# Optimization experiments

Hardware: AMD Instinct MI355X
Metric: run time of the kernel (lower is better)

Reference implementation:

```python
import jax, jax.numpy as jnp
import numpy as np
from jax import lax

D_MODEL = 1024
N_HEADS = 16
HEAD_DIM = D_MODEL // N_HEADS
B, S = 4, 2048
EPS = 1e-5


def setup_inputs() -> dict:
    key = jax.random.key(0)
    ks = jax.random.split(key, 8)
    sc = 1.0 / np.sqrt(D_MODEL)
    return {
        "x": jax.random.normal(ks[0], (B, S, D_MODEL), dtype=jnp.float32),
        "Wq": jax.random.normal(ks[1], (D_MODEL, D_MODEL), dtype=jnp.float32) * sc,
        "Wk": jax.random.normal(ks[2], (D_MODEL, D_MODEL), dtype=jnp.float32) * sc,
        "Wv": jax.random.normal(ks[3], (D_MODEL, D_MODEL), dtype=jnp.float32) * sc,
        "Wa": jax.random.normal(ks[4], (D_MODEL, N_HEADS), dtype=jnp.float32) * sc,
        "ba": jnp.zeros((N_HEADS,), dtype=jnp.float32),
        "Wb": jax.random.normal(ks[5], (D_MODEL, N_HEADS), dtype=jnp.float32) * sc,
        "bb": jnp.zeros((N_HEADS,), dtype=jnp.float32),
        "Wg": jax.random.normal(ks[6], (D_MODEL, D_MODEL), dtype=jnp.float32) * sc,
        "Wo": jax.random.normal(ks[7], (D_MODEL, D_MODEL), dtype=jnp.float32) * sc,
        "g_norm": jnp.ones((D_MODEL,), dtype=jnp.float32),
    }


def _l2_normalize(v, eps=1e-12):
    # F.normalize(dim=-1) in float32
    v32 = v.astype(jnp.float32)
    n = jnp.sqrt(jnp.sum(v32 * v32, axis=-1, keepdims=True))
    return (v32 / jnp.maximum(n, eps)).astype(v.dtype)


def _rmsnorm(x, w):
    x32 = x.astype(jnp.float32)
    rms = lax.rsqrt(jnp.mean(x32 * x32, axis=-1, keepdims=True) + EPS)
    return (x32 * rms).astype(x.dtype) * w


def reference(x, Wq, Wk, Wv, Wa, ba, Wb, bb, Wg, Wo, g_norm):
    batch, seq_len, d_model = x.shape
    H, hd = N_HEADS, HEAD_DIM
    residual_input = x

    # projections -> [B, S, H, hd]
    q = (x @ Wq).reshape(batch, seq_len, H, hd)
    k = (x @ Wk).reshape(batch, seq_len, H, hd)
    v = (x @ Wv).reshape(batch, seq_len, H, hd)
    q = _l2_normalize(q)
    k = _l2_normalize(k)

    alpha = jax.nn.sigmoid(x @ Wa + ba)  # [B, S, H]
    beta = jax.nn.sigmoid(x @ Wb + bb)   # [B, S, H]

    # time-major for scan: [S, B, H, ...]
    qt = jnp.moveaxis(q, 1, 0)
    kt = jnp.moveaxis(k, 1, 0)
    vt = jnp.moveaxis(v, 1, 0)
    at = jnp.moveaxis(alpha, 1, 0)
    bt = jnp.moveaxis(beta, 1, 0)

    state0 = jnp.zeros((batch, H, hd, hd), dtype=x.dtype)

    def step(state, inp):
        q_t, k_t, v_t, a_t, b_t = inp  # [B,H,hd], [B,H]
        pred = jnp.einsum('bhde,bhd->bhe', state, k_t)
        error = v_t - pred
        update = jnp.einsum('bhe,bhd->bhde', b_t[..., None] * error, k_t)
        state = a_t[..., None, None] * state + update
        out = jnp.einsum('bhde,bhd->bhe', state, q_t)
        return state, out

    _, ys = lax.scan(step, state0, (qt, kt, vt, at, bt))  # ys: [S,B,H,hd]
    y = jnp.moveaxis(ys, 0, 1).reshape(batch, seq_len, d_model)

    gate = jax.nn.silu(residual_input @ Wg)
    y = _rmsnorm(y, g_norm) * gate
    return y @ Wo


if __name__ == "__main__":
    out = reference(**setup_inputs())
    print(out.shape)
```

## Files before the change

kernel.cpp:

```cpp
#include <hip/hip_runtime.h>
#include <hip/hip_bf16.h>
#include <math.h>

typedef __attribute__((ext_vector_type(8))) short bf16x8s;
typedef __attribute__((ext_vector_type(4))) float f32x4;

#define SEQ 2048
#define NTOK 8192
#define NQKV 3200

static __device__ __forceinline__ float bf2f(unsigned short u) {
  union { unsigned int i; float f; } c; c.i = ((unsigned int)u) << 16; return c.f;
}
static __device__ __forceinline__ unsigned short f2bf(float f) {
  union { float f; unsigned int i; } c; c.f = f;
  unsigned int x = c.i;
  return (unsigned short)((x + 0x7FFFu + ((x >> 16) & 1u)) >> 16);
}

static __device__ __forceinline__ float red8(float x) {
  union { float f; int i; } c, d;
  c.f = x; d.i = __builtin_amdgcn_update_dpp(0, c.i, 0xB1, 0xF, 0xF, true); x += d.f;
  c.f = x; d.i = __builtin_amdgcn_update_dpp(0, c.i, 0x4E, 0xF, 0xF, true); x += d.f;
  c.f = x; d.i = __builtin_amdgcn_update_dpp(0, c.i, 0x141, 0xF, 0xF, true); x += d.f;
  return x;
}
static __device__ __forceinline__ float red16(float x) {
  union { float f; int i; } c, d;
  c.f = x; d.i = __builtin_amdgcn_update_dpp(0, c.i, 0xB1, 0xF, 0xF, true); x += d.f;
  c.f = x; d.i = __builtin_amdgcn_update_dpp(0, c.i, 0x4E, 0xF, 0xF, true); x += d.f;
  c.f = x; d.i = __builtin_amdgcn_update_dpp(0, c.i, 0x141, 0xF, 0xF, true); x += d.f;
  c.f = x; d.i = __builtin_amdgcn_update_dpp(0, c.i, 0x140, 0xF, 0xF, true); x += d.f;
  return x;
}

__global__ __launch_bounds__(256) void castx_k(const float* __restrict__ in,
                                               unsigned short* __restrict__ out, int n4) {
  int i = blockIdx.x * 256 + threadIdx.x;
  if (i >= n4) return;
  float4 v = ((const float4*)in)[i];
  ushort4 o;
  o.x = f2bf(v.x); o.y = f2bf(v.y); o.z = f2bf(v.z); o.w = f2bf(v.w);
  ((ushort4*)out)[i] = o;
}

__global__ void transpose_k(const float* __restrict__ in,
                            unsigned short* __restrict__ out, int R, int C) {
  __shared__ unsigned short tile[32][33];
  int c0 = blockIdx.x * 32, r0 = blockIdx.y * 32;
  int tx = threadIdx.x, ty = threadIdx.y;
  for (int i = ty; i < 32; i += 8)
    tile[i][tx] = f2bf(in[(size_t)(r0 + i) * C + c0 + tx]);
  __syncthreads();
  for (int i = ty; i < 32; i += 8)
    out[(size_t)(c0 + i) * R + r0 + tx] = tile[tx][i];
}

__global__ void build_wabT(const float* __restrict__ Wa,
                           const float* __restrict__ Wb,
                           unsigned short* __restrict__ rows) {
  int i = blockIdx.x * 256 + threadIdx.x;
  int j = i >> 10, k = i & 1023;
  float v = 0.f;
  if (j < 16) v = Wa[k * 16 + j];
  else if (j < 32) v = Wb[k * 16 + (j - 16)];
  rows[(size_t)j * 1024 + k] = f2bf(v);
}

template<int MODE>
__global__ __launch_bounds__(256) void gemm_bt(const unsigned short* __restrict__ A,
                                               const unsigned short* __restrict__ Bt,
                                               void* __restrict__ Cv,
                                               int M, int N, int K,
                                               const float* __restrict__ ba,
                                               const float* __restrict__ bbp,
                                               float* __restrict__ alphaF,
                                               float* __restrict__ betaF) {
  __shared__ __align__(16) unsigned short As[128 * 32];
  __shared__ __align__(16) unsigned short Bs[128 * 32];
  int tiles_n = N >> 7;
  int tm = blockIdx.x / tiles_n, tn = blockIdx.x % tiles_n;
  int m0 = tm << 7, n0 = tn << 7;
  int tid = threadIdx.x;
  int wave = tid >> 6, lane = tid & 63;
  int wm = wave >> 1, wn = wave & 1;
  int r = lane & 15, qd = lane >> 4;
  int lr = lane >> 2, lc = lane & 3;

  f32x4 acc[4][4];
#pragma unroll
  for (int mi = 0; mi < 4; mi++)
#pragma unroll
    for (int ni = 0; ni < 4; ni++) acc[mi][ni] = (f32x4){0.f, 0.f, 0.f, 0.f};

  for (int k0 = 0; k0 < K; k0 += 32) {
#pragma unroll
    for (int gi = 0; gi < 2; ++gi) {
      int g = wave + gi * 4;
      int row = g * 16 + lr;
      const unsigned short* ga = A + (size_t)(m0 + row) * K + k0 + lc * 8;
      const unsigned short* gb = Bt + (size_t)(n0 + row) * K + k0 + lc * 8;
      __builtin_amdgcn_global_load_lds(
          (const __attribute__((address_space(1))) unsigned int*)ga,
          (__attribute__((address_space(3))) unsigned int*)(As + g * 512 + lane * 8),
          16, 0, 0);
      __builtin_amdgcn_global_load_lds(
          (const __attribute__((address_space(1))) unsigned int*)gb,
          (__attribute__((address_space(3))) unsigned int*)(Bs + g * 512 + lane * 8),
          16, 0, 0);
    }
    __syncthreads();
    bf16x8s af[4], bfr[4];
#pragma unroll
    for (int mi = 0; mi < 4; mi++)
      af[mi] = *(const bf16x8s*)&As[(wm * 64 + mi * 16 + r) * 32 + qd * 8];
#pragma unroll
    for (int ni = 0; ni < 4; ni++)
      bfr[ni] = *(const bf16x8s*)&Bs[(wn * 64 + ni * 16 + r) * 32 + qd * 8];
#pragma unroll
    for (int mi = 0; mi < 4; mi++)
#pragma unroll
      for (int ni = 0; ni < 4; ni++)
        acc[mi][ni] = __builtin_amdgcn_mfma_f32_16x16x32_bf16(af[mi], bfr[ni], acc[mi][ni], 0, 0, 0);
    __syncthreads();
  }

  bool qk = (MODE == 2) && (n0 < 2048);
#pragma unroll
  for (int mi = 0; mi < 4; mi++) {
    f32x4 sc = (f32x4){1.f, 1.f, 1.f, 1.f};
    if (qk) {
      f32x4 ss = acc[mi][0] * acc[mi][0] + acc[mi][1] * acc[mi][1]
               + acc[mi][2] * acc[mi][2] + acc[mi][3] * acc[mi][3];
#pragma unroll
      for (int cc = 0; cc < 4; cc++) {
        float s = red16(ss[cc]);
        sc[cc] = 1.f / fmaxf(sqrtf(s), 1e-12f);
      }
    }
#pragma unroll
    for (int ni = 0; ni < 4; ni++)
#pragma unroll
      for (int reg = 0; reg < 4; reg++) {
        int m = m0 + wm * 64 + mi * 16 + qd * 4 + reg;
        int n = n0 + wn * 64 + ni * 16 + r;
        float a = acc[mi][ni][reg];
        if (MODE == 0) ((unsigned short*)Cv)[(size_t)m * N + n] = f2bf(a);
        else if (MODE == 1) ((float*)Cv)[(size_t)m * N + n] = a;
        else {
          if (qk) a *= sc[reg];
          if (n < 3072) ((unsigned short*)Cv)[(size_t)m * 3072 + n] = f2bf(a);
          else if (n < 3104) {
            int j = n - 3072;
            float bias = (j < 16) ? ba[j] : bbp[j - 16];
            float s = 1.f / (1.f + expf(-(a + bias)));
            if (j < 16) alphaF[(size_t)m * 16 + j] = s;
            else        betaF[(size_t)m * 16 + (j - 16)] = s;
          }
        }
      }
  }
}

#define TC 32
#define NCH (SEQ / TC)
#define LK 0
#define LQ 2048
#define LV 4096
#define LABQ 4352
#define SBUF 4480

static __device__ __forceinline__ void unpack8(uint4 v, float* f) {
  f[0] = bf2f((unsigned short)(v.x & 0xffff)); f[1] = bf2f((unsigned short)(v.x >> 16));
  f[2] = bf2f((unsigned short)(v.y & 0xffff)); f[3] = bf2f((unsigned short)(v.y >> 16));
  f[4] = bf2f((unsigned short)(v.z & 0xffff)); f[5] = bf2f((unsigned short)(v.z >> 16));
  f[6] = bf2f((unsigned short)(v.w & 0xffff)); f[7] = bf2f((unsigned short)(v.w >> 16));
}

struct Pref { uint4 k8[4], q8[4], v8; float ab; };

static __device__ __forceinline__ Pref scan_load(const unsigned short* __restrict__ qkv,
                                                 const float* __restrict__ alphaF,
                                                 const float* __restrict__ betaF,
                                                 int b, int h, int ec, int t0, int tid) {
  Pref p; p.v8 = (uint4){0, 0, 0, 0};
  const unsigned short* base = qkv + (size_t)(b * SEQ + t0) * 3072 + h * 64;
#pragma unroll
  for (int j = 0; j < 4; ++j) {
    int idx = j * 64 + tid;
    int t = idx >> 3, seg = idx & 7;
    p.q8[j] = *(const uint4*)(base + (size_t)t * 3072 + seg * 8);
    p.k8[j] = *(const uint4*)(base + (size_t)t * 3072 + 1024 + seg * 8);
  }
  if (tid < 32) {
    p.v8 = *(const uint4*)(base + (size_t)tid * 3072 + 2048 + ec * 8);
    p.ab = alphaF[(size_t)(b * SEQ + t0 + tid) * 16 + h];
  } else {
    p.ab = betaF[(size_t)(b * SEQ + t0 + (tid - 32)) * 16 + h];
  }
  return p;
}

static __device__ __forceinline__ void scan_store(float* __restrict__ buf, const Pref& p, int tid) {
#pragma unroll
  for (int j = 0; j < 4; ++j) {
    int idx = j * 64 + tid;
    int t = idx >> 3, seg = idx & 7;
    float kf[8], qf[8];
    unpack8(p.k8[j], kf);
    unpack8(p.q8[j], qf);
    *(float4*)&buf[LK + t * 64 + seg * 8]     = (float4){kf[0], kf[1], kf[2], kf[3]};
    *(float4*)&buf[LK + t * 64 + seg * 8 + 4] = (float4){kf[4], kf[5], kf[6], kf[7]};
    *(float4*)&buf[LQ + t * 64 + seg * 8]     = (float4){qf[0], qf[1], qf[2], qf[3]};
    *(float4*)&buf[LQ + t * 64 + seg * 8 + 4] = (float4){qf[4], qf[5], qf[6], qf[7]};
    float s = kf[0]*qf[0] + kf[1]*qf[1] + kf[2]*qf[2] + kf[3]*qf[3]
            + kf[4]*qf[4] + kf[5]*qf[5] + kf[6]*qf[6] + kf[7]*qf[7];
    s = red8(s);
    if ((tid & 7) == 0) buf[LABQ + t * 4 + 2] = s;
  }
  if (tid < 32) {
    float vf[8];
    unpack8(p.v8, vf);
    *(float4*)&buf[LV + tid * 8]     = (float4){vf[0], vf[1], vf[2], vf[3]};
    *(float4*)&buf[LV + tid * 8 + 4] = (float4){vf[4], vf[5], vf[6], vf[7]};
    buf[LABQ + tid * 4 + 0] = p.ab;
  } else {
    buf[LABQ + (tid - 32) * 4 + 1] = p.ab;
  }
}

__global__ __launch_bounds__(64) void scan_k(const unsigned short* __restrict__ qkv,
                                             const float* __restrict__ alphaF,
                                             const float* __restrict__ betaF,
                                             unsigned short* __restrict__ y) {
  __shared__ float sm[2 * SBUF];
  int bh = blockIdx.x >> 3, ec = blockIdx.x & 7;
  int b = bh >> 4, h = bh & 15;
  int tid = threadIdx.x;
  int el = tid >> 3, g = tid & 3 + 0;
  g = tid & 7;

  float S0 = 0.f, S1 = 0.f, S2 = 0.f, S3 = 0.f;
  float S4 = 0.f, S5 = 0.f, S6 = 0.f, S7 = 0.f;

  Pref p = scan_load(qkv, alphaF, betaF, b, h, ec, 0, tid);
  scan_store(sm, p, tid);
  __syncthreads();

  unsigned short* yb = y + (size_t)(b * SEQ) * 1024 + h * 64 + ec * 8 + el;

  for (int c = 0; c < NCH; ++c) {
    if (c + 1 < NCH)
      p = scan_load(qkv, alphaF, betaF, b, h, ec, (c + 1) * TC, tid);

    const float* bb = sm + (c & 1) * SBUF;
    float4 rk0[2], rk1[2], rq0[2], rq1[2], rabq[2];
    float rve[2];
#pragma unroll
    for (int i = 0; i < 2; ++i) {
      rk0[i] = *(const float4*)&bb[LK + i * 64 + g * 8];
      rk1[i] = *(const float4*)&bb[LK + i * 64 + g * 8 + 4];
      rq0[i] = *(const float4*)&bb[LQ + i * 64 + g * 8];
      rq1[i] = *(const float4*)&bb[LQ + i * 64 + g * 8 + 4];
      rve[i] = bb[LV + i * 8 + el];
      rabq[i] = *(const float4*)&bb[LABQ + i * 4];
    }
    float yo[TC];
#pragma unroll
    for (int t = 0; t < TC; ++t) {
      const int sl = t & 1;
      float4 k0 = rk0[sl], k1 = rk1[sl], q0 = rq0[sl], q1 = rq1[sl];
      float4 abq = rabq[sl];
      float ve = rve[sl];
      float at = abq.x, bt = abq.y, kqv = abq.z;
      float btve = bt * ve;
      float pr = ((S0*k0.x + S1*k0.y) + (S2*k0.z + S3*k0.w))
               + ((S4*k1.x + S5*k1.y) + (S6*k1.z + S7*k1.w));
      float qs = ((S0*q0.x + S1*q0.y) + (S2*q0.z + S3*q0.w))
               + ((S4*q1.x + S5*q1.y) + (S6*q1.z + S7*q1.w));
      pr = red8(pr);
      qs = red8(qs);
      float be = btve - bt * pr;
      S0 = at*S0 + be*k0.x;  S1 = at*S1 + be*k0.y;
      S2 = at*S2 + be*k0.z;  S3 = at*S3 + be*k0.w;
      S4 = at*S4 + be*k1.x;  S5 = at*S5 + be*k1.y;
      S6 = at*S6 + be*k1.z;  S7 = at*S7 + be*k1.w;
      yo[t] = at * qs + be * kqv;
      if (t + 2 < TC) {
        const int tn = t + 2;
        rk0[sl] = *(const float4*)&bb[LK + tn * 64 + g * 8];
        rk1[sl] = *(const float4*)&bb[LK + tn * 64 + g * 8 + 4];
        rq0[sl] = *(const float4*)&bb[LQ + tn * 64 + g * 8];
        rq1[sl] = *(const float4*)&bb[LQ + tn * 64 + g * 8 + 4];
        rve[sl] = bb[LV + tn * 8 + el];
        rabq[sl] = *(const float4*)&bb[LABQ + tn * 4];
      }
    }
    if (g == 0) {
#pragma unroll
      for (int t = 0; t < TC; ++t)
        yb[(size_t)(c * TC + t) * 1024] = f2bf(yo[t]);
    }
    if (c + 1 < NCH) {
      scan_store(sm + ((c + 1) & 1) * SBUF, p, tid);
      __syncthreads();
    }
  }
}

__global__ __launch_bounds__(256) void rmsgate_k(const unsigned short* __restrict__ y,
                                                 const unsigned short* __restrict__ gl,
                                                 const float* __restrict__ gnorm,
                                                 unsigned short* __restrict__ z) {
  __shared__ float red[4];
  int row = blockIdx.x, tid = threadIdx.x;
  size_t base = (size_t)row * 1024 + tid * 4;
  uint2 yv = *(const uint2*)&y[base];
  float f0 = bf2f((unsigned short)(yv.x & 0xffff)), f1 = bf2f((unsigned short)(yv.x >> 16));
  float f2 = bf2f((unsigned short)(yv.y & 0xffff)), f3 = bf2f((unsigned short)(yv.y >> 16));
  float ss = f0 * f0 + f1 * f1 + f2 * f2 + f3 * f3;
#pragma unroll
  for (int s = 1; s < 64; s <<= 1) ss += __shfl_xor(ss, s);
  if ((tid & 63) == 0) red[tid >> 6] = ss;
  __syncthreads();
  ss = red[0] + red[1] + red[2] + red[3];
  float rms = rsqrtf(ss * (1.0f / 1024.0f) + 1e-5f);
  uint2 gv = *(const uint2*)&gl[base];
  float4 gn = *(const float4*)&gnorm[tid * 4];
  float g[4] = {bf2f((unsigned short)(gv.x & 0xffff)), bf2f((unsigned short)(gv.x >> 16)),
                bf2f((unsigned short)(gv.y & 0xffff)), bf2f((unsigned short)(gv.y >> 16))};
  float gnv[4] = {gn.x, gn.y, gn.z, gn.w};
  float fv[4] = {f0, f1, f2, f3};
  unsigned short o[4];
#pragma unroll
  for (int jj = 0; jj < 4; jj++) {
    float gate = g[jj] / (1.f + expf(-g[jj]));
    o[jj] = f2bf(fv[jj] * rms * gnv[jj] * gate);
  }
  uint2 ov;
  ov.x = (unsigned int)o[0] | ((unsigned int)o[1] << 16);
  ov.y = (unsigned int)o[2] | ((unsigned int)o[3] << 16);
  *(uint2*)&z[base] = ov;
}

extern "C" void kernel_launch(void* const* d_in, const int* in_sizes, int n_in,
                              void* d_out, int out_size, void* d_ws, size_t ws_size,
                              hipStream_t stream) {
  const float* x     = (const float*)d_in[0];
  const float* Wq    = (const float*)d_in[1];
  const float* Wk    = (const float*)d_in[2];
  const float* Wv    = (const float*)d_in[3];
  const float* Wa    = (const float*)d_in[4];
  const float* ba    = (const float*)d_in[5];
  const float* Wb    = (const float*)d_in[6];
  const float* bb    = (const float*)d_in[7];
  const float* Wg    = (const float*)d_in[8];
  const float* Wo    = (const float*)d_in[9];
  const float* gnorm = (const float*)d_in[10];
  float* out = (float*)d_out;

  unsigned short* xbf    = (unsigned short*)d_ws;
  unsigned short* Bt_qkv = xbf + (size_t)NTOK * 1024;
  unsigned short* Bt_g   = Bt_qkv + (size_t)NQKV * 1024;
  unsigned short* Bt_o   = Bt_g + (size_t)1024 * 1024;
  unsigned short* qkv    = Bt_o + (size_t)1024 * 1024;
  unsigned short* gatelin= qkv + (size_t)NTOK * 3072;
  unsigned short* ybuf   = gatelin + (size_t)NTOK * 1024;
  float* alphaF          = (float*)(ybuf + (size_t)NTOK * 1024);
  float* betaF           = alphaF + (size_t)NTOK * 16;
  unsigned short* zbuf   = xbf;

  castx_k<<<NTOK * 1024 / 4 / 256, 256, 0, stream>>>(x, xbf, NTOK * 1024 / 4);
  dim3 tb(32, 8);
  transpose_k<<<dim3(32, 32), tb, 0, stream>>>(Wq, Bt_qkv, 1024, 1024);
  transpose_k<<<dim3(32, 32), tb, 0, stream>>>(Wk, Bt_qkv + (size_t)1024 * 1024, 1024, 1024);
  transpose_k<<<dim3(32, 32), tb, 0, stream>>>(Wv, Bt_qkv + (size_t)2048 * 1024, 1024, 1024);
  transpose_k<<<dim3(32, 32), tb, 0, stream>>>(Wg, Bt_g, 1024, 1024);
  transpose_k<<<dim3(32, 32), tb, 0, stream>>>(Wo, Bt_o, 1024, 1024);
  build_wabT<<<512, 256, 0, stream>>>(Wa, Wb, Bt_qkv + (size_t)3072 * 1024);

  gemm_bt<2><<<(NTOK / 128) * (NQKV / 128), 256, 0, stream>>>(
      xbf, Bt_qkv, qkv, NTOK, NQKV, 1024, ba, bb, alphaF, betaF);
  gemm_bt<0><<<(NTOK / 128) * (1024 / 128), 256, 0, stream>>>(
      xbf, Bt_g, gatelin, NTOK, 1024, 1024, nullptr, nullptr, nullptr, nullptr);
  scan_k<<<512, 64, 0, stream>>>(qkv, alphaF, betaF, ybuf);
  rmsgate_k<<<NTOK, 256, 0, stream>>>(ybuf, gatelin, gnorm, zbuf);
  gemm_bt<1><<<(NTOK / 128) * (1024 / 128), 256, 0, stream>>>(
      zbuf, Bt_o, out, NTOK, 1024, 1024, nullptr, nullptr, nullptr, nullptr);
}
```

Measured before the change: 614.6 us.

## Lookahead-restructure delta-rule scan to take reductions off the recurrence critical path

Rewrites the per-step recurrence so the state-times-k and state-times-q dot products for step t+1 are computed from the state before step t's update. They are then corrected using precomputed k_{t}·k_{t+1} and k_{t}·q_{t+1} scalars. This lets the cross-lane DPP reductions overlap with the state update instead of serializing it. It also folds beta into v when staging, packs the state into float2 vectors to allow packed FMA, and precomputes the extra dot products in shared memory, which needs an extra barrier and slightly larger buffers. The algebra introduces small floating-point reassociation differences.

```diff
diff --git a/kernel.cpp b/kernel.cpp
--- a/kernel.cpp
+++ b/kernel.cpp
@@ -4,6 +4,7 @@
 
 typedef __attribute__((ext_vector_type(8))) short bf16x8s;
 typedef __attribute__((ext_vector_type(4))) float f32x4;
+typedef __attribute__((ext_vector_type(2))) float f32x2;
 
 #define SEQ 2048
 #define NTOK 8192
@@ -168,7 +169,7 @@
 #define LQ 2048
 #define LV 4096
 #define LABQ 4352
-#define SBUF 4480
+#define SBUF 4608
 
 static __device__ __forceinline__ void unpack8(uint4 v, float* f) {
   f[0] = bf2f((unsigned short)(v.x & 0xffff)); f[1] = bf2f((unsigned short)(v.x >> 16));
@@ -199,6 +200,20 @@
     p.ab = betaF[(size_t)(b * SEQ + t0 + (tid - 32)) * 16 + h];
   }
   return p;
+}
+
+static __device__ __forceinline__ float dot8s(float4 a0, float4 a1, float4 b0, float4 b1) {
+  return ((a0.x * b0.x + a0.y * b0.y) + (a0.z * b0.z + a0.w * b0.w))
+       + ((a1.x * b1.x + a1.y * b1.y) + (a1.z * b1.z + a1.w * b1.w));
+}
+
+static __device__ __forceinline__ float dot8v(f32x2 S01, f32x2 S23, f32x2 S45, f32x2 S67,
+                                              float4 x0, float4 x1) {
+  f32x2 X01 = {x0.x, x0.y}, X23 = {x0.z, x0.w}, X45 = {x1.x, x1.y}, X67 = {x1.z, x1.w};
+  f32x2 t1 = S01 * X01 + S23 * X23;
+  f32x2 t2 = S45 * X45 + S67 * X67;
+  f32x2 s = t1 + t2;
+  return s.x + s.y;
 }
 
 static __device__ __forceinline__ void scan_store(float* __restrict__ buf, const Pref& p, int tid) {
@@ -216,18 +231,50 @@
     float s = kf[0]*qf[0] + kf[1]*qf[1] + kf[2]*qf[2] + kf[3]*qf[3]
             + kf[4]*qf[4] + kf[5]*qf[5] + kf[6]*qf[6] + kf[7]*qf[7];
     s = red8(s);
-    if ((tid & 7) == 0) buf[LABQ + t * 4 + 2] = s;
-  }
+    if ((tid & 7) == 0) buf[LABQ + t * 8 + 2] = s;
+  }
+  float btv = __shfl(p.ab, tid | 32);
   if (tid < 32) {
     float vf[8];
     unpack8(p.v8, vf);
-    *(float4*)&buf[LV + tid * 8]     = (float4){vf[0], vf[1], vf[2], vf[3]};
-    *(float4*)&buf[LV + tid * 8 + 4] = (float4){vf[4], vf[5], vf[6], vf[7]};
-    buf[LABQ + tid * 4 + 0] = p.ab;
+    *(float4*)&buf[LV + tid * 8]     = (float4){btv*vf[0], btv*vf[1], btv*vf[2], btv*vf[3]};
+    *(float4*)&buf[LV + tid * 8 + 4] = (float4){btv*vf[4], btv*vf[5], btv*vf[6], btv*vf[7]};
+    buf[LABQ + tid * 8 + 0] = p.ab;
   } else {
-    buf[LABQ + (tid - 32) * 4 + 1] = p.ab;
-  }
-}
+    buf[LABQ + (tid - 32) * 8 + 1] = p.ab;
+  }
+  __syncthreads();
+#pragma unroll
+  for (int j = 0; j < 4; ++j) {
+    int idx = j * 64 + tid;
+    int t = idx >> 3, seg = idx & 7;
+    float4 kc0 = *(const float4*)&buf[LK + t * 64 + seg * 8];
+    float4 kc1 = *(const float4*)&buf[LK + t * 64 + seg * 8 + 4];
+    float4 qc0 = *(const float4*)&buf[LQ + t * 64 + seg * 8];
+    float4 qc1 = *(const float4*)&buf[LQ + t * 64 + seg * 8 + 4];
+    float4 kp0 = (float4){0.f, 0.f, 0.f, 0.f}, kp1 = kp0;
+    if (t > 0) {
+      kp0 = *(const float4*)&buf[LK + (t - 1) * 64 + seg * 8];
+      kp1 = *(const float4*)&buf[LK + (t - 1) * 64 + seg * 8 + 4];
+    }
+    float skk = red8(dot8s(kp0, kp1, kc0, kc1));
+    float skq = red8(dot8s(kp0, kp1, qc0, qc1));
+    if ((tid & 7) == 0) {
+      buf[LABQ + t * 8 + 3] = skk;
+      buf[LABQ + t * 8 + 4] = skq;
+    }
+  }
+}
+
+#define LOADSLOT(BB, I, TT) do {                                        \
+    rk0[I]  = *(const float4*)&(BB)[LK + (TT) * 64 + g * 8];            \
+    rk1[I]  = *(const float4*)&(BB)[LK + (TT) * 64 + g * 8 + 4];        \
+    rq0[I]  = *(const float4*)&(BB)[LQ + (TT) * 64 + g * 8];            \
+    rq1[I]  = *(const float4*)&(BB)[LQ + (TT) * 64 + g * 8 + 4];        \
+    rabq[I] = *(const float4*)&(BB)[LABQ + (TT) * 8];                   \
+    rkq1[I] = (BB)[LABQ + (TT) * 8 + 4];                                \
+    rbv[I]  = (BB)[LV + (TT) * 8 + el];                                 \
+  } while (0)
 
 __global__ __launch_bounds__(64) void scan_k(const unsigned short* __restrict__ qkv,
                                              const float* __restrict__ alphaF,
@@ -237,16 +284,21 @@
   int bh = blockIdx.x >> 3, ec = blockIdx.x & 7;
   int b = bh >> 4, h = bh & 15;
   int tid = threadIdx.x;
-  int el = tid >> 3, g = tid & 3 + 0;
-  g = tid & 7;
-
-  float S0 = 0.f, S1 = 0.f, S2 = 0.f, S3 = 0.f;
-  float S4 = 0.f, S5 = 0.f, S6 = 0.f, S7 = 0.f;
+  int el = tid >> 3;
+  int g = tid & 7;
+
+  f32x2 S01 = {0.f, 0.f}, S23 = {0.f, 0.f}, S45 = {0.f, 0.f}, S67 = {0.f, 0.f};
 
   Pref p = scan_load(qkv, alphaF, betaF, b, h, ec, 0, tid);
   scan_store(sm, p, tid);
   __syncthreads();
 
+  float4 rk0[2], rk1[2], rq0[2], rq1[2], rabq[2];
+  float rkq1[2], rbv[2];
+  LOADSLOT(sm, 0, 0);
+  LOADSLOT(sm, 1, 1);
+  float uP = 0.f, wP = 0.f, cP = 0.f, aP = 0.f;
+
   unsigned short* yb = y + (size_t)(b * SEQ) * 1024 + h * 64 + ec * 8 + el;
 
   for (int c = 0; c < NCH; ++c) {
@@ -254,47 +306,34 @@
       p = scan_load(qkv, alphaF, betaF, b, h, ec, (c + 1) * TC, tid);
 
     const float* bb = sm + (c & 1) * SBUF;
-    float4 rk0[2], rk1[2], rq0[2], rq1[2], rabq[2];
-    float rve[2];
-#pragma unroll
-    for (int i = 0; i < 2; ++i) {
-      rk0[i] = *(const float4*)&bb[LK + i * 64 + g * 8];
-      rk1[i] = *(const float4*)&bb[LK + i * 64 + g * 8 + 4];
-      rq0[i] = *(const float4*)&bb[LQ + i * 64 + g * 8];
-      rq1[i] = *(const float4*)&bb[LQ + i * 64 + g * 8 + 4];
-      rve[i] = bb[LV + i * 8 + el];
-      rabq[i] = *(const float4*)&bb[LABQ + i * 4];
-    }
     float yo[TC];
 #pragma unroll
     for (int t = 0; t < TC; ++t) {
       const int sl = t & 1;
-      float4 k0 = rk0[sl], k1 = rk1[sl], q0 = rq0[sl], q1 = rq1[sl];
+      float4 k0 = rk0[sl], k1 = rk1[sl];
       float4 abq = rabq[sl];
-      float ve = rve[sl];
-      float at = abq.x, bt = abq.y, kqv = abq.z;
-      float btve = bt * ve;
-      float pr = ((S0*k0.x + S1*k0.y) + (S2*k0.z + S3*k0.w))
-               + ((S4*k1.x + S5*k1.y) + (S6*k1.z + S7*k1.w));
-      float qs = ((S0*q0.x + S1*q0.y) + (S2*q0.z + S3*q0.w))
-               + ((S4*q1.x + S5*q1.y) + (S6*q1.z + S7*q1.w));
-      pr = red8(pr);
-      qs = red8(qs);
-      float be = btve - bt * pr;
-      S0 = at*S0 + be*k0.x;  S1 = at*S1 + be*k0.y;
-      S2 = at*S2 + be*k0.z;  S3 = at*S3 + be*k0.w;
-      S4 = at*S4 + be*k1.x;  S5 = at*S5 + be*k1.y;
-      S6 = at*S6 + be*k1.z;  S7 = at*S7 + be*k1.w;
-      yo[t] = at * qs + be * kqv;
-      if (t + 2 < TC) {
-        const int tn = t + 2;
-        rk0[sl] = *(const float4*)&bb[LK + tn * 64 + g * 8];
-        rk1[sl] = *(const float4*)&bb[LK + tn * 64 + g * 8 + 4];
-        rq0[sl] = *(const float4*)&bb[LQ + tn * 64 + g * 8];
-        rq1[sl] = *(const float4*)&bb[LQ + tn * 64 + g * 8 + 4];
-        rve[sl] = bb[LV + tn * 8 + el];
-        rabq[sl] = *(const float4*)&bb[LABQ + tn * 4];
+      float kq1v = rkq1[sl], bv = rbv[sl];
+      float a = abq.x, bt = abq.y, kq0 = abq.z, kk = abq.w;
+      if (t + 2 < TC) LOADSLOT(bb, sl, t + 2);
+      float uN = 0.f, wN = 0.f;
+      if (t + 1 < TC) {
+        const int so = sl ^ 1;
+        uN = red8(dot8v(S01, S23, S45, S67, rk0[so], rk1[so]));
+        wN = red8(dot8v(S01, S23, S45, S67, rq0[so], rq1[so]));
       }
+      float pr = fmaf(aP, uP, cP * kk);
+      float qs = fmaf(aP, wP, cP * kq1v);
+      float cc = fmaf(-bt, pr, bv);
+      yo[t] = fmaf(a, qs, cc * kq0);
+      f32x2 a2; a2.x = a; a2.y = a;
+      f32x2 c2; c2.x = cc; c2.y = cc;
+      f32x2 aS0 = a2 * S01, aS1 = a2 * S23, aS2 = a2 * S45, aS3 = a2 * S67;
+      f32x2 K01 = {k0.x, k0.y}, K23 = {k0.z, k0.w}, K45 = {k1.x, k1.y}, K67 = {k1.z, k1.w};
+      S01 = c2 * K01 + aS0;
+      S23 = c2 * K23 + aS1;
+      S45 = c2 * K45 + aS2;
+      S67 = c2 * K67 + aS3;
+      uP = uN; wP = wN; cP = cc; aP = a;
     }
     if (g == 0) {
 #pragma unroll
@@ -302,8 +341,14 @@
         yb[(size_t)(c * TC + t) * 1024] = f2bf(yo[t]);
     }
     if (c + 1 < NCH) {
-      scan_store(sm + ((c + 1) & 1) * SBUF, p, tid);
+      float* nb = sm + ((c + 1) & 1) * SBUF;
+      scan_store(nb, p, tid);
       __syncthreads();
+      LOADSLOT(nb, 0, 0);
+      LOADSLOT(nb, 1, 1);
+      uP = red8(dot8v(S01, S23, S45, S67, rk0[0], rk1[0]));
+      wP = red8(dot8v(S01, S23, S45, S67, rq0[0], rq1[0]));
+      cP = 0.f; aP = 1.f;
     }
   }
 }
```

New measurement: 647.8 us. +5.4%, slower.

## Replace sequential delta-rule scan with chunked MFMA-based chunkwise scan

Applied to the files above, without the earlier changes.

Replaces the per-token recurrent scan, which used 512 single-wave blocks each owning 8 value columns, with a chunkwise formulation. Each 512-thread block owns one (batch, head) pair and processes 32-token chunks. Within a chunk, Gram matrices, state projections and state updates run as bf16 MFMA ops, with the state split into hi/lo bf16 halves to keep precision. Only a small 32x32 triangular solve stays sequential in one wave. Loads use async global-to-LDS copies and are double-buffered, but the grid drops to 64 blocks, which risks low GPU occupancy and adds precision risk from bf16 splitting and division by cumulative alpha products.

```diff
diff --git a/kernel.cpp b/kernel.cpp
--- a/kernel.cpp
+++ b/kernel.cpp
@@ -18,13 +18,6 @@
   return (unsigned short)((x + 0x7FFFu + ((x >> 16) & 1u)) >> 16);
 }
 
-static __device__ __forceinline__ float red8(float x) {
-  union { float f; int i; } c, d;
-  c.f = x; d.i = __builtin_amdgcn_update_dpp(0, c.i, 0xB1, 0xF, 0xF, true); x += d.f;
-  c.f = x; d.i = __builtin_amdgcn_update_dpp(0, c.i, 0x4E, 0xF, 0xF, true); x += d.f;
-  c.f = x; d.i = __builtin_amdgcn_update_dpp(0, c.i, 0x141, 0xF, 0xF, true); x += d.f;
-  return x;
-}
 static __device__ __forceinline__ float red16(float x) {
   union { float f; int i; } c, d;
   c.f = x; d.i = __builtin_amdgcn_update_dpp(0, c.i, 0xB1, 0xF, 0xF, true); x += d.f;
@@ -162,148 +155,328 @@
   }
 }
 
-#define TC 32
-#define NCH (SEQ / TC)
-#define LK 0
-#define LQ 2048
-#define LV 4096
-#define LABQ 4352
-#define SBUF 4480
-
-static __device__ __forceinline__ void unpack8(uint4 v, float* f) {
-  f[0] = bf2f((unsigned short)(v.x & 0xffff)); f[1] = bf2f((unsigned short)(v.x >> 16));
-  f[2] = bf2f((unsigned short)(v.y & 0xffff)); f[3] = bf2f((unsigned short)(v.y >> 16));
-  f[4] = bf2f((unsigned short)(v.z & 0xffff)); f[5] = bf2f((unsigned short)(v.z >> 16));
-  f[6] = bf2f((unsigned short)(v.w & 0xffff)); f[7] = bf2f((unsigned short)(v.w >> 16));
-}
-
-struct Pref { uint4 k8[4], q8[4], v8; float ab; };
-
-static __device__ __forceinline__ Pref scan_load(const unsigned short* __restrict__ qkv,
-                                                 const float* __restrict__ alphaF,
-                                                 const float* __restrict__ betaF,
-                                                 int b, int h, int ec, int t0, int tid) {
-  Pref p; p.v8 = (uint4){0, 0, 0, 0};
-  const unsigned short* base = qkv + (size_t)(b * SEQ + t0) * 3072 + h * 64;
-#pragma unroll
-  for (int j = 0; j < 4; ++j) {
-    int idx = j * 64 + tid;
-    int t = idx >> 3, seg = idx & 7;
-    p.q8[j] = *(const uint4*)(base + (size_t)t * 3072 + seg * 8);
-    p.k8[j] = *(const uint4*)(base + (size_t)t * 3072 + 1024 + seg * 8);
-  }
-  if (tid < 32) {
-    p.v8 = *(const uint4*)(base + (size_t)tid * 3072 + 2048 + ec * 8);
-    p.ab = alphaF[(size_t)(b * SEQ + t0 + tid) * 16 + h];
-  } else {
-    p.ab = betaF[(size_t)(b * SEQ + t0 + (tid - 32)) * 16 + h];
-  }
-  return p;
-}
-
-static __device__ __forceinline__ void scan_store(float* __restrict__ buf, const Pref& p, int tid) {
-#pragma unroll
-  for (int j = 0; j < 4; ++j) {
-    int idx = j * 64 + tid;
-    int t = idx >> 3, seg = idx & 7;
-    float kf[8], qf[8];
-    unpack8(p.k8[j], kf);
-    unpack8(p.q8[j], qf);
-    *(float4*)&buf[LK + t * 64 + seg * 8]     = (float4){kf[0], kf[1], kf[2], kf[3]};
-    *(float4*)&buf[LK + t * 64 + seg * 8 + 4] = (float4){kf[4], kf[5], kf[6], kf[7]};
-    *(float4*)&buf[LQ + t * 64 + seg * 8]     = (float4){qf[0], qf[1], qf[2], qf[3]};
-    *(float4*)&buf[LQ + t * 64 + seg * 8 + 4] = (float4){qf[4], qf[5], qf[6], qf[7]};
-    float s = kf[0]*qf[0] + kf[1]*qf[1] + kf[2]*qf[2] + kf[3]*qf[3]
-            + kf[4]*qf[4] + kf[5]*qf[5] + kf[6]*qf[6] + kf[7]*qf[7];
-    s = red8(s);
-    if ((tid & 7) == 0) buf[LABQ + t * 4 + 2] = s;
-  }
-  if (tid < 32) {
-    float vf[8];
-    unpack8(p.v8, vf);
-    *(float4*)&buf[LV + tid * 8]     = (float4){vf[0], vf[1], vf[2], vf[3]};
-    *(float4*)&buf[LV + tid * 8 + 4] = (float4){vf[4], vf[5], vf[6], vf[7]};
-    buf[LABQ + tid * 4 + 0] = p.ab;
-  } else {
-    buf[LABQ + (tid - 32) * 4 + 1] = p.ab;
-  }
-}
-
-__global__ __launch_bounds__(64) void scan_k(const unsigned short* __restrict__ qkv,
-                                             const float* __restrict__ alphaF,
-                                             const float* __restrict__ betaF,
-                                             unsigned short* __restrict__ y) {
-  __shared__ float sm[2 * SBUF];
-  int bh = blockIdx.x >> 3, ec = blockIdx.x & 7;
-  int b = bh >> 4, h = bh & 15;
-  int tid = threadIdx.x;
-  int el = tid >> 3, g = tid & 3 + 0;
-  g = tid & 7;
-
-  float S0 = 0.f, S1 = 0.f, S2 = 0.f, S3 = 0.f;
-  float S4 = 0.f, S5 = 0.f, S6 = 0.f, S7 = 0.f;
-
-  Pref p = scan_load(qkv, alphaF, betaF, b, h, ec, 0, tid);
-  scan_store(sm, p, tid);
+#define D_OFF_STHI 0
+#define D_OFF_STLO 8192
+#define D_OFF_K    16384
+#define D_OFF_Q    24576
+#define D_OFF_V    32768
+#define D_OFF_KT   40960
+#define D_OFF_MT   45056
+#define D_OFF_GBF  53248
+#define D_OFF_CTHI 57344
+#define D_OFF_CTLO 67584
+#define D_OFF_W    77824
+#define D_OFF_U    86016
+#define D_OFF_AB   102400
+#define D_LDS_SIZE 104512
+
+static __device__ __forceinline__ float rdlane(float v, int i) {
+  return __int_as_float(__builtin_amdgcn_readlane(__float_as_int(v), i));
+}
+
+__global__ __launch_bounds__(512, 2) void dscan_k(const unsigned short* __restrict__ qkv,
+                                                  const float* __restrict__ alphaF,
+                                                  const float* __restrict__ betaF,
+                                                  unsigned short* __restrict__ y) {
+  extern __shared__ char smem[];
+  const int bh = blockIdx.x;
+  const int b = bh >> 4, h = bh & 15;
+  const int tid = threadIdx.x, wid = tid >> 6, lane = tid & 63;
+  const int r = lane & 15, qd = lane >> 4;
+
+  float* abf = (float*)(smem + D_OFF_AB);
+
+  auto stage_jobs = [&](int cn) {
+    int buf = cn & 1;
+    int tok0 = b * SEQ + cn * 32;
+    int row = lane >> 3, s8 = lane & 7;
+    int sx = ((s8 ^ (row & 7)) * 8);
+    {
+      int p = (wid < 4) ? wid : wid - 4;
+      int colbase = (wid < 4) ? (1024 + h * 64) : (h * 64);
+      int off = (wid < 4) ? D_OFF_K : D_OFF_Q;
+      const unsigned short* src = qkv + (size_t)(tok0 + p * 8 + row) * 3072 + colbase + sx;
+      unsigned short* dst = (unsigned short*)(smem + off + buf * 4096 + p * 1024) + lane * 8;
+      __builtin_amdgcn_global_load_lds(
+          (const __attribute__((address_space(1))) unsigned int*)src,
+          (__attribute__((address_space(3))) unsigned int*)dst, 16, 0, 0);
+    }
+    if (wid < 4) {
+      int p = wid;
+      const unsigned short* src = qkv + (size_t)(tok0 + p * 8 + row) * 3072 + 2048 + h * 64 + sx;
+      unsigned short* dst = (unsigned short*)(smem + D_OFF_V + buf * 4096 + p * 1024) + lane * 8;
+      __builtin_amdgcn_global_load_lds(
+          (const __attribute__((address_space(1))) unsigned int*)src,
+          (__attribute__((address_space(3))) unsigned int*)dst, 16, 0, 0);
+    }
+  };
+
+  auto ab_compute = [&](int cn) {
+    int t = lane & 31;
+    int tok = b * SEQ + cn * 32 + t;
+    float av = alphaF[(size_t)tok * 16 + h];
+    float bv = betaF[(size_t)tok * 16 + h];
+    float p = av;
+#pragma unroll
+    for (int s = 1; s < 32; s <<= 1) {
+      float o = __shfl_up(p, s, 32);
+      if ((lane & 31) >= s) p *= o;
+    }
+    float ep = __shfl_up(p, 1, 32);
+    if ((lane & 31) == 0) ep = 1.f;
+    float* ap = abf + (cn & 3) * 132;
+    if (lane < 32) {
+      ap[0 + t] = ep;
+      ap[32 + t] = p;
+      ap[64 + t] = 1.0f / p;
+      if (t == 31) ap[128] = p;
+    } else {
+      ap[96 + t] = bv;
+    }
+  };
+
+  auto gram_do = [&](int cn) {
+    if (wid < 3 || wid > 6) return;
+    int buf = cn & 1;
+    const char* Kn = smem + D_OFF_K + buf * 4096;
+    const char* Qn = smem + D_OFF_Q + buf * 4096;
+    const float* ap = abf + (cn & 3) * 132;
+    bool kk = (wid <= 4);
+    int g0 = (kk ? (wid - 3) : (wid - 5)) * 2;
+#pragma unroll
+    for (int j = 0; j < 2; ++j) {
+      int g = g0 + j, gi = g >> 1, gt = g & 1;
+      f32x4 acc = (f32x4){0.f, 0.f, 0.f, 0.f};
+#pragma unroll
+      for (int ks = 0; ks < 2; ++ks) {
+        int o = ks * 64 + qd * 16;
+        bf16x8s af = *(const bf16x8s*)(Kn + (gi * 16 + r) * 128 + (o ^ ((r & 7) << 4)));
+        bf16x8s bf = kk
+            ? *(const bf16x8s*)(Kn + (gt * 16 + r) * 128 + (o ^ ((r & 7) << 4)))
+            : *(const bf16x8s*)(Qn + (gt * 16 + r) * 128 + (o ^ ((r & 7) << 4)));
+        acc = __builtin_amdgcn_mfma_f32_16x16x32_bf16(af, bf, acc, 0, 0, 0);
+      }
+      int tl = gt * 16 + r;
+      f32x4 ei4 = *(const f32x4*)&ap[64 + gi * 16 + qd * 4];
+      if (kk) {
+        float bt = ap[96 + tl], ept = ap[0 + tl];
+        float* Mtp = (float*)(smem + D_OFF_MT + buf * 4096);
+#pragma unroll
+        for (int reg = 0; reg < 4; ++reg) {
+          int i = gi * 16 + qd * 4 + reg;
+          Mtp[i * 32 + tl] = (i < tl) ? bt * ept * ei4[reg] * acc[reg] : 0.f;
+        }
+      } else {
+        float et = ap[32 + tl];
+        unsigned short* Gp = (unsigned short*)(smem + D_OFF_GBF + buf * 2048);
+#pragma unroll
+        for (int reg = 0; reg < 4; ++reg) {
+          int i = gi * 16 + qd * 4 + reg;
+          float v = (i <= tl) ? et * ei4[reg] * acc[reg] : 0.f;
+          Gp[tl * 32 + i] = f2bf(v);
+        }
+      }
+    }
+  };
+
+  float sreg[8];
+#pragma unroll
+  for (int i = 0; i < 8; ++i) sreg[i] = 0.f;
+
+  {
+    uint4 z = (uint4){0u, 0u, 0u, 0u};
+    *(uint4*)(smem + D_OFF_STHI + tid * 16) = z;
+    *(uint4*)(smem + D_OFF_STLO + tid * 16) = z;
+  }
+  stage_jobs(0);
+  if (wid == 0) ab_compute(0);
+  else if (wid == 1) ab_compute(1);
   __syncthreads();
-
-  unsigned short* yb = y + (size_t)(b * SEQ) * 1024 + h * 64 + ec * 8 + el;
-
-  for (int c = 0; c < NCH; ++c) {
-    if (c + 1 < NCH)
-      p = scan_load(qkv, alphaF, betaF, b, h, ec, (c + 1) * TC, tid);
-
-    const float* bb = sm + (c & 1) * SBUF;
-    float4 rk0[2], rk1[2], rq0[2], rq1[2], rabq[2];
-    float rve[2];
-#pragma unroll
-    for (int i = 0; i < 2; ++i) {
-      rk0[i] = *(const float4*)&bb[LK + i * 64 + g * 8];
-      rk1[i] = *(const float4*)&bb[LK + i * 64 + g * 8 + 4];
-      rq0[i] = *(const float4*)&bb[LQ + i * 64 + g * 8];
-      rq1[i] = *(const float4*)&bb[LQ + i * 64 + g * 8 + 4];
-      rve[i] = bb[LV + i * 8 + el];
-      rabq[i] = *(const float4*)&bb[LABQ + i * 4];
-    }
-    float yo[TC];
-#pragma unroll
-    for (int t = 0; t < TC; ++t) {
-      const int sl = t & 1;
-      float4 k0 = rk0[sl], k1 = rk1[sl], q0 = rq0[sl], q1 = rq1[sl];
-      float4 abq = rabq[sl];
-      float ve = rve[sl];
-      float at = abq.x, bt = abq.y, kqv = abq.z;
-      float btve = bt * ve;
-      float pr = ((S0*k0.x + S1*k0.y) + (S2*k0.z + S3*k0.w))
-               + ((S4*k1.x + S5*k1.y) + (S6*k1.z + S7*k1.w));
-      float qs = ((S0*q0.x + S1*q0.y) + (S2*q0.z + S3*q0.w))
-               + ((S4*q1.x + S5*q1.y) + (S6*q1.z + S7*q1.w));
-      pr = red8(pr);
-      qs = red8(qs);
-      float be = btve - bt * pr;
-      S0 = at*S0 + be*k0.x;  S1 = at*S1 + be*k0.y;
-      S2 = at*S2 + be*k0.z;  S3 = at*S3 + be*k0.w;
-      S4 = at*S4 + be*k1.x;  S5 = at*S5 + be*k1.y;
-      S6 = at*S6 + be*k1.z;  S7 = at*S7 + be*k1.w;
-      yo[t] = at * qs + be * kqv;
-      if (t + 2 < TC) {
-        const int tn = t + 2;
-        rk0[sl] = *(const float4*)&bb[LK + tn * 64 + g * 8];
-        rk1[sl] = *(const float4*)&bb[LK + tn * 64 + g * 8 + 4];
-        rq0[sl] = *(const float4*)&bb[LQ + tn * 64 + g * 8];
-        rq1[sl] = *(const float4*)&bb[LQ + tn * 64 + g * 8 + 4];
-        rve[sl] = bb[LV + tn * 8 + el];
-        rabq[sl] = *(const float4*)&bb[LABQ + tn * 4];
-      }
-    }
-    if (g == 0) {
-#pragma unroll
-      for (int t = 0; t < TC; ++t)
-        yb[(size_t)(c * TC + t) * 1024] = f2bf(yo[t]);
-    }
-    if (c + 1 < NCH) {
-      scan_store(sm + ((c + 1) & 1) * SBUF, p, tid);
-      __syncthreads();
+  gram_do(0);
+  __syncthreads();
+
+  const char* SThi = smem + D_OFF_STHI;
+  const char* STlo = smem + D_OFF_STLO;
+
+  for (int c = 0; c < 64; ++c) {
+    const int cbuf = c & 1, cs = c & 3;
+    if (c + 1 < 64) stage_jobs(c + 1);
+    {
+      int tt = wid >> 2, te = wid & 3;
+      const char* Kc = smem + D_OFF_K + cbuf * 4096;
+      f32x4 acc = (f32x4){0.f, 0.f, 0.f, 0.f};
+#pragma unroll
+      for (int ks = 0; ks < 2; ++ks) {
+        int o = ks * 64 + qd * 16;
+        bf16x8s af = *(const bf16x8s*)(Kc + (tt * 16 + r) * 128 + (o ^ ((r & 7) << 4)));
+        bf16x8s bhv = *(const bf16x8s*)(SThi + (te * 16 + r) * 128 + (o ^ ((r & 7) << 4)));
+        bf16x8s blv = *(const bf16x8s*)(STlo + (te * 16 + r) * 128 + (o ^ ((r & 7) << 4)));
+        acc = __builtin_amdgcn_mfma_f32_16x16x32_bf16(af, bhv, acc, 0, 0, 0);
+        acc = __builtin_amdgcn_mfma_f32_16x16x32_bf16(af, blv, acc, 0, 0, 0);
+      }
+      float* Wp = (float*)(smem + D_OFF_W);
+#pragma unroll
+      for (int reg = 0; reg < 4; ++reg)
+        Wp[(tt * 16 + qd * 4 + reg) * 64 + te * 16 + r] = acc[reg];
+    }
+    if (c >= 1) {
+      int cc = c - 1, buf = cc & 1;
+      int ty = wid >> 2, te = wid & 3;
+      const char* Gp = smem + D_OFF_GBF + buf * 2048;
+      bf16x8s af = *(const bf16x8s*)(Gp + (ty * 16 + r) * 64 + qd * 16);
+      bf16x8s bhv = *(const bf16x8s*)(smem + D_OFF_CTHI + buf * 5120 + (te * 16 + r) * 80 + qd * 16);
+      bf16x8s blv = *(const bf16x8s*)(smem + D_OFF_CTLO + buf * 5120 + (te * 16 + r) * 80 + qd * 16);
+      f32x4 acc = (f32x4){0.f, 0.f, 0.f, 0.f};
+      acc = __builtin_amdgcn_mfma_f32_16x16x32_bf16(af, bhv, acc, 0, 0, 0);
+      acc = __builtin_amdgcn_mfma_f32_16x16x32_bf16(af, blv, acc, 0, 0, 0);
+      const float* Up = (const float*)(smem + D_OFF_U + buf * 8192);
+      f32x4 e4 = *(const f32x4*)&abf[(cc & 3) * 132 + 32 + ty * 16 + qd * 4];
+#pragma unroll
+      for (int reg = 0; reg < 4; ++reg) {
+        int t = ty * 16 + qd * 4 + reg, e = te * 16 + r;
+        float yv = fmaf(e4[reg], Up[t * 64 + e], acc[reg]);
+        y[(size_t)(b * SEQ + cc * 32 + t) * 1024 + h * 64 + e] = f2bf(yv);
+      }
+    }
+    __syncthreads();
+
+    if (wid == 0) {
+      const float* Wp = (const float*)(smem + D_OFF_W);
+      const char* Vb = smem + D_OFF_V + cbuf * 4096;
+      const float* ap = abf + cs * 132;
+      float vb = ap[96 + (lane & 31)];
+      float vep = ap[0 + (lane & 31)];
+      float d_[32], r_[32];
+#pragma unroll
+      for (int i = 0; i < 32; ++i) r_[i] = 0.f;
+#pragma unroll
+      for (int i = 0; i < 32; ++i) {
+        float w = Wp[i * 64 + lane];
+        unsigned short vx = *(const unsigned short*)(Vb + (i * 128 + ((lane * 2) ^ ((i & 7) << 4))));
+        d_[i] = rdlane(vb, i) * fmaf(-rdlane(vep, i), w, bf2f(vx));
+      }
+      const float* Mtp = (const float*)(smem + D_OFF_MT + cbuf * 4096);
+#pragma unroll
+      for (int i = 0; i < 32; ++i) {
+        float cv = d_[i] - r_[i];
+        d_[i] = cv;
+#pragma unroll
+        for (int cb4 = 0; cb4 < 8; ++cb4) {
+          if (cb4 * 4 + 3 > i) {
+            f32x4 m4 = *(const f32x4*)&Mtp[i * 32 + cb4 * 4];
+            r_[cb4 * 4 + 0] = fmaf(m4[0], cv, r_[cb4 * 4 + 0]);
+            r_[cb4 * 4 + 1] = fmaf(m4[1], cv, r_[cb4 * 4 + 1]);
+            r_[cb4 * 4 + 2] = fmaf(m4[2], cv, r_[cb4 * 4 + 2]);
+            r_[cb4 * 4 + 3] = fmaf(m4[3], cv, r_[cb4 * 4 + 3]);
+          }
+        }
+      }
+      unsigned int ph[16], pl[16];
+#pragma unroll
+      for (int j = 0; j < 16; ++j) {
+        unsigned short h0 = f2bf(d_[2 * j]), h1 = f2bf(d_[2 * j + 1]);
+        ph[j] = (unsigned int)h0 | ((unsigned int)h1 << 16);
+        float l0 = d_[2 * j] - bf2f(h0), l1 = d_[2 * j + 1] - bf2f(h1);
+        pl[j] = (unsigned int)f2bf(l0) | ((unsigned int)f2bf(l1) << 16);
+      }
+      char* Ch = smem + D_OFF_CTHI + cbuf * 5120 + lane * 80;
+      char* Cl = smem + D_OFF_CTLO + cbuf * 5120 + lane * 80;
+#pragma unroll
+      for (int k = 0; k < 4; ++k) {
+        *(uint4*)(Ch + k * 16) = (uint4){ph[4 * k], ph[4 * k + 1], ph[4 * k + 2], ph[4 * k + 3]};
+        *(uint4*)(Cl + k * 16) = (uint4){pl[4 * k], pl[4 * k + 1], pl[4 * k + 2], pl[4 * k + 3]};
+      }
+    } else {
+      if (wid <= 4) {
+        const char* Qc = smem + D_OFF_Q + cbuf * 4096;
+        float* Up = (float*)(smem + D_OFF_U + cbuf * 8192);
+#pragma unroll
+        for (int j = 0; j < 2; ++j) {
+          int u = (wid - 1) * 2 + j, tu = u >> 2, te = u & 3;
+          f32x4 acc = (f32x4){0.f, 0.f, 0.f, 0.f};
+#pragma unroll
+          for (int ks = 0; ks < 2; ++ks) {
+            int o = ks * 64 + qd * 16;
+            bf16x8s af = *(const bf16x8s*)(Qc + (tu * 16 + r) * 128 + (o ^ ((r & 7) << 4)));
+            bf16x8s bhv = *(const bf16x8s*)(SThi + (te * 16 + r) * 128 + (o ^ ((r & 7) << 4)));
+            bf16x8s blv = *(const bf16x8s*)(STlo + (te * 16 + r) * 128 + (o ^ ((r & 7) << 4)));
+            acc = __builtin_amdgcn_mfma_f32_16x16x32_bf16(af, bhv, acc, 0, 0, 0);
+            acc = __builtin_amdgcn_mfma_f32_16x16x32_bf16(af, blv, acc, 0, 0, 0);
+          }
+#pragma unroll
+          for (int reg = 0; reg < 4; ++reg)
+            Up[(tu * 16 + qd * 4 + reg) * 64 + te * 16 + r] = acc[reg];
+        }
+      }
+      if (c + 1 < 64) gram_do(c + 1);
+      if (wid == 7) {
+        const float* ap = abf + cs * 132;
+        float vei = ap[64 + (lane & 31)];
+        float e31 = ap[128];
+        const char* Kc = smem + D_OFF_K + cbuf * 4096;
+        unsigned short* KT = (unsigned short*)(smem + D_OFF_KT);
+        unsigned int pk[16];
+#pragma unroll
+        for (int i = 0; i < 32; ++i) {
+          unsigned short kv = *(const unsigned short*)(Kc + (i * 128 + ((lane * 2) ^ ((i & 7) << 4))));
+          float f = bf2f(kv) * (e31 * rdlane(vei, i));
+          unsigned short o = f2bf(f);
+          if (i & 1) pk[i >> 1] |= ((unsigned int)o << 16);
+          else       pk[i >> 1] = o;
+        }
+#pragma unroll
+        for (int k = 0; k < 4; ++k)
+          *(uint4*)((char*)KT + lane * 64 + k * 16) =
+              (uint4){pk[4 * k], pk[4 * k + 1], pk[4 * k + 2], pk[4 * k + 3]};
+      }
+      if (wid == 2 && c + 2 < 64) ab_compute(c + 2);
+    }
+    __syncthreads();
+
+    {
+      float e31 = abf[cs * 132 + 128];
+      const char* KT = smem + D_OFF_KT;
+#pragma unroll
+      for (int j = 0; j < 2; ++j) {
+        int s = wid * 2 + j, td = s >> 2, te = s & 3;
+        bf16x8s af = *(const bf16x8s*)(KT + (td * 16 + r) * 64 + qd * 16);
+        bf16x8s bhv = *(const bf16x8s*)(smem + D_OFF_CTHI + cbuf * 5120 + (te * 16 + r) * 80 + qd * 16);
+        bf16x8s blv = *(const bf16x8s*)(smem + D_OFF_CTLO + cbuf * 5120 + (te * 16 + r) * 80 + qd * 16);
+        f32x4 acc = (f32x4){0.f, 0.f, 0.f, 0.f};
+        acc = __builtin_amdgcn_mfma_f32_16x16x32_bf16(af, bhv, acc, 0, 0, 0);
+        acc = __builtin_amdgcn_mfma_f32_16x16x32_bf16(af, blv, acc, 0, 0, 0);
+#pragma unroll
+        for (int reg = 0; reg < 4; ++reg) {
+          int d = td * 16 + qd * 4 + reg, e = te * 16 + r;
+          float sv = fmaf(e31, sreg[j * 4 + reg], acc[reg]);
+          sreg[j * 4 + reg] = sv;
+          unsigned short hi = f2bf(sv);
+          float lo = sv - bf2f(hi);
+          *(unsigned short*)(smem + D_OFF_STHI + e * 128 + ((d * 2) ^ ((e & 7) << 4))) = hi;
+          *(unsigned short*)(smem + D_OFF_STLO + e * 128 + ((d * 2) ^ ((e & 7) << 4))) = f2bf(lo);
+        }
+      }
+    }
+    __syncthreads();
+  }
+
+  {
+    int cc = 63, buf = cc & 1;
+    int ty = wid >> 2, te = wid & 3;
+    const char* Gp = smem + D_OFF_GBF + buf * 2048;
+    bf16x8s af = *(const bf16x8s*)(Gp + (ty * 16 + r) * 64 + qd * 16);
+    bf16x8s bhv = *(const bf16x8s*)(smem + D_OFF_CTHI + buf * 5120 + (te * 16 + r) * 80 + qd * 16);
+    bf16x8s blv = *(const bf16x8s*)(smem + D_OFF_CTLO + buf * 5120 + (te * 16 + r) * 80 + qd * 16);
+    f32x4 acc = (f32x4){0.f, 0.f, 0.f, 0.f};
+    acc = __builtin_amdgcn_mfma_f32_16x16x32_bf16(af, bhv, acc, 0, 0, 0);
+    acc = __builtin_amdgcn_mfma_f32_16x16x32_bf16(af, blv, acc, 0, 0, 0);
+    const float* Up = (const float*)(smem + D_OFF_U + buf * 8192);
+    f32x4 e4 = *(const f32x4*)&abf[(cc & 3) * 132 + 32 + ty * 16 + qd * 4];
+#pragma unroll
+    for (int reg = 0; reg < 4; ++reg) {
+      int t = ty * 16 + qd * 4 + reg, e = te * 16 + r;
+      float yv = fmaf(e4[reg], Up[t * 64 + e], acc[reg]);
+      y[(size_t)(b * SEQ + cc * 32 + t) * 1024 + h * 64 + e] = f2bf(yv);
     }
   }
 }
@@ -370,6 +543,13 @@
   float* betaF           = alphaF + (size_t)NTOK * 16;
   unsigned short* zbuf   = xbf;
 
+  static int dscan_inited = 0;
+  if (!dscan_inited) {
+    hipFuncSetAttribute((const void*)dscan_k,
+                        hipFuncAttributeMaxDynamicSharedMemorySize, D_LDS_SIZE);
+    dscan_inited = 1;
+  }
+
   castx_k<<<NTOK * 1024 / 4 / 256, 256, 0, stream>>>(x, xbf, NTOK * 1024 / 4);
   dim3 tb(32, 8);
   transpose_k<<<dim3(32, 32), tb, 0, stream>>>(Wq, Bt_qkv, 1024, 1024);
@@ -383,7 +563,7 @@
       xbf, Bt_qkv, qkv, NTOK, NQKV, 1024, ba, bb, alphaF, betaF);
   gemm_bt<0><<<(NTOK / 128) * (1024 / 128), 256, 0, stream>>>(
       xbf, Bt_g, gatelin, NTOK, 1024, 1024, nullptr, nullptr, nullptr, nullptr);
-  scan_k<<<512, 64, 0, stream>>>(qkv, alphaF, betaF, ybuf);
+  dscan_k<<<64, 512, D_LDS_SIZE, stream>>>(qkv, alphaF, betaF, ybuf);
   rmsgate_k<<<NTOK, 256, 0, stream>>>(ybuf, gatelin, gnorm, zbuf);
   gemm_bt<1><<<(NTOK / 128) * (1024 / 128), 256, 0, stream>>>(
       zbuf, Bt_o, out, NTOK, 1024, 1024, nullptr, nullptr, nullptr, nullptr);
```

Result: faster. 538.3 us (-12.4%).
